# Kernel optimization log

Hardware: AMD Instinct MI355X
Metric: run time of the kernel (lower is better)

Reference implementation:

```python
import math
import jax, jax.numpy as jnp
import numpy as np

N_HEAD = 16

def setup_inputs() -> dict:
    key = jax.random.key(0)
    ks = jax.random.split(key, 3)
    B, T, C = 2, 2048, 1024
    x = jax.random.normal(ks[0], (B, T, C), dtype=jnp.float32)
    W_attn = jax.random.normal(ks[1], (3 * C, C), dtype=jnp.float32) * (1.0 / math.sqrt(C))
    b_attn = jnp.zeros((3 * C,), dtype=jnp.float32)
    W_proj = jax.random.normal(ks[2], (C, C), dtype=jnp.float32) * (1.0 / math.sqrt(C))
    b_proj = jnp.zeros((C,), dtype=jnp.float32)
    return {"x": x, "W_attn": W_attn, "b_attn": b_attn, "W_proj": W_proj, "b_proj": b_proj}

def reference(x, W_attn, b_attn, W_proj, b_proj):
    B, T, C = x.shape
    H = N_HEAD
    Dh = C // H
    qkv = x @ W_attn.T + b_attn                      # [B,T,3C]
    q, k, v = jnp.split(qkv, 3, axis=-1)
    q = q.reshape(B, T, H, Dh).transpose(0, 2, 1, 3)  # [B,H,T,Dh]
    k = k.reshape(B, T, H, Dh).transpose(0, 2, 1, 3)
    v = v.reshape(B, T, H, Dh).transpose(0, 2, 1, 3)
    att = jnp.einsum('bhqd,bhkd->bhqk', q, k) * (1.0 / math.sqrt(Dh))
    # ALiBi-style RPE: bias[h, r, c] = -(r - c) * 2^(-8/H * (h+1)) for c <= r, 0 above diag
    rows = jnp.arange(T)[:, None]
    cols = jnp.arange(T)[None, :]
    dist = jnp.minimum((cols - rows).astype(jnp.float32), 0.0)  # [T,T]
    slopes = 2.0 ** (-8.0 / H * (jnp.arange(H, dtype=jnp.float32) + 1.0))  # [H]
    att = att + slopes[None, :, None, None] * dist[None, None]
    causal = cols <= rows                              # [T,T]
    att = jnp.where(causal[None, None], att, -jnp.inf)
    att = jax.nn.softmax(att, axis=-1)                 # dropout p=0.0 -> identity
    y = jnp.einsum('bhqk,bhkd->bhqd', att, v)          # [B,H,T,Dh]
    y = y.transpose(0, 2, 1, 3).reshape(B, T, C)
    y = y @ W_proj.T + b_proj
    return y
```

## Files before the change

### kernel.cpp

```cpp
#include <hip/hip_runtime.h>

typedef __bf16 bf16x8 __attribute__((ext_vector_type(8)));
typedef __bf16 bf16x4 __attribute__((ext_vector_type(4)));
typedef float  f32x4  __attribute__((ext_vector_type(4)));
typedef float  f32x16 __attribute__((ext_vector_type(16)));

#define TSEQ 2048
#define CDIM 1024
#define NHEAD 16
#define DH 64
#define SCALE2 0.1803368801111137f

__device__ __forceinline__ void gl_lds16(const void* g, void* l) {
  __builtin_amdgcn_global_load_lds(
      (const __attribute__((address_space(1))) unsigned int*)g,
      (__attribute__((address_space(3))) unsigned int*)l, 16, 0, 0);
}

__device__ __forceinline__ float fexp2(float x) { return __builtin_amdgcn_exp2f(x); }

__device__ __forceinline__ unsigned cvtpk(float a, float b) {
  unsigned r;
  asm("v_cvt_pk_bf16_f32 %0, %1, %2" : "=v"(r) : "v"(a), "v"(b));
  return r;
}
__device__ __forceinline__ void permswap(unsigned& x, unsigned& y) {
  asm("v_permlane32_swap_b32 %0, %1" : "+v"(x), "+v"(y));
}

__device__ __forceinline__ float tsum16(const f32x16& s) {
  float a0 = s[0] + s[1], a1 = s[2] + s[3], a2 = s[4] + s[5], a3 = s[6] + s[7];
  float a4 = s[8] + s[9], a5 = s[10] + s[11], a6 = s[12] + s[13], a7 = s[14] + s[15];
  float b0 = a0 + a1, b1 = a2 + a3, b2 = a4 + a5, b3 = a6 + a7;
  return (b0 + b1) + (b2 + b3);
}

__global__ __launch_bounds__(256) void cvt_bf16_all(
    const float* __restrict__ x, const float* __restrict__ wa,
    const float* __restrict__ wp, __bf16* __restrict__ xb,
    __bf16* __restrict__ wab, __bf16* __restrict__ wpb) {
  int i = blockIdx.x * 256 + threadIdx.x;
  const float* in;
  __bf16* out;
  int off;
  if (i < 524288)      { in = x;  out = xb;  off = i; }
  else if (i < 917504) { in = wa; out = wab; off = i - 524288; }
  else                 { in = wp; out = wpb; off = i - 917504; }
  const float4* p = (const float4*)(in + (size_t)off * 8);
  float4 a = p[0], b = p[1];
  bf16x8 r;
  r[0] = (__bf16)a.x; r[1] = (__bf16)a.y; r[2] = (__bf16)a.z; r[3] = (__bf16)a.w;
  r[4] = (__bf16)b.x; r[5] = (__bf16)b.y; r[6] = (__bf16)b.z; r[7] = (__bf16)b.w;
  *(bf16x8*)(out + (size_t)off * 8) = r;
}

__global__ __launch_bounds__(256) void gemm_qkv(
    const __bf16* __restrict__ A, const __bf16* __restrict__ Bw,
    const float* __restrict__ bias,
    __bf16* __restrict__ q_buf, __bf16* __restrict__ k_buf,
    __bf16* __restrict__ vT_buf, int K) {
  __shared__ alignas(16) __bf16 lda[128 * 64];
  __shared__ alignas(16) __bf16 ldb[128 * 64];
  const int tid = threadIdx.x;
  const int lane = tid & 63, wid = tid >> 6;
  const int wm = wid >> 1, wn = wid & 1;
  const int row0 = blockIdx.y * 128, col0 = blockIdx.x * 128;
  f32x4 acc[4][4] = {};

  const int srow = lane >> 3;
  const int scb = ((lane & 7) ^ (lane >> 3)) * 16;

  for (int k0 = 0; k0 < K; k0 += 64) {
#pragma unroll
    for (int j = 0; j < 4; ++j) {
      int blk = j * 4 + wid;
      int r = blk * 8 + srow;
      char* la = (char*)lda + blk * 1024;
      char* lb = (char*)ldb + blk * 1024;
      gl_lds16((const char*)(A + (size_t)(row0 + r) * K + k0) + scb, la);
      gl_lds16((const char*)(Bw + (size_t)(col0 + r) * K + k0) + scb, lb);
    }
    __syncthreads();
#pragma unroll
    for (int kk = 0; kk < 2; ++kk) {
      const int sl = (((kk << 2) | (lane >> 4)) ^ (lane & 7)) * 16;
      bf16x8 af[4], bfr[4];
#pragma unroll
      for (int m = 0; m < 4; ++m)
        af[m] = *(const bf16x8*)((const char*)lda +
                                 (wm * 64 + m * 16 + (lane & 15)) * 128 + sl);
#pragma unroll
      for (int n = 0; n < 4; ++n)
        bfr[n] = *(const bf16x8*)((const char*)ldb +
                                  (wn * 64 + n * 16 + (lane & 15)) * 128 + sl);
#pragma unroll
      for (int m = 0; m < 4; ++m)
#pragma unroll
        for (int n = 0; n < 4; ++n)
          acc[m][n] = __builtin_amdgcn_mfma_f32_16x16x32_bf16(af[m], bfr[n], acc[m][n], 0, 0, 0);
    }
    __syncthreads();
  }
#pragma unroll
  for (int m = 0; m < 4; ++m) {
#pragma unroll
    for (int n = 0; n < 4; ++n) {
#pragma unroll
      for (int i = 0; i < 4; ++i) {
        int r = row0 + wm * 64 + m * 16 + (lane >> 4) * 4 + i;
        int c = col0 + wn * 64 + n * 16 + (lane & 15);
        float v = acc[m][n][i] + bias[c];
        int bb = r >> 11, t = r & 2047;
        int sec = c >> 10, cc = c & 1023;
        int hh = cc >> 6, d = cc & 63;
        size_t bh = (size_t)bb * NHEAD + hh;
        if (sec == 0)      q_buf[(bh * TSEQ + (size_t)t) * DH + d] = (__bf16)(v * SCALE2);
        else if (sec == 1) k_buf[(bh * TSEQ + (size_t)t) * DH + d] = (__bf16)v;
        else               vT_buf[(bh * DH + (size_t)d) * TSEQ + t] = (__bf16)v;
      }
    }
  }
}

__global__ __launch_bounds__(256) void gemm_proj(
    const __bf16* __restrict__ A, const __bf16* __restrict__ Bw,
    const float* __restrict__ bias, float* __restrict__ outf) {
  const int K = CDIM, N = CDIM;
  __shared__ alignas(16) __bf16 lda[64 * 64];
  __shared__ alignas(16) __bf16 ldb[128 * 64];
  const int tid = threadIdx.x;
  const int lane = tid & 63, wid = tid >> 6;
  const int row0 = blockIdx.y * 64, col0 = blockIdx.x * 128;
  f32x4 acc[4][2] = {};

  const int srow = lane >> 3;
  const int scb = ((lane & 7) ^ (lane >> 3)) * 16;

  for (int k0 = 0; k0 < K; k0 += 64) {
#pragma unroll
    for (int j = 0; j < 2; ++j) {
      int blk = j * 4 + wid;
      gl_lds16((const char*)(A + (size_t)(row0 + blk * 8 + srow) * K + k0) + scb,
               (char*)lda + blk * 1024);
    }
#pragma unroll
    for (int j = 0; j < 4; ++j) {
      int blk = j * 4 + wid;
      gl_lds16((const char*)(Bw + (size_t)(col0 + blk * 8 + srow) * K + k0) + scb,
               (char*)ldb + blk * 1024);
    }
    __syncthreads();
#pragma unroll
    for (int kk = 0; kk < 2; ++kk) {
      const int sl = (((kk << 2) | (lane >> 4)) ^ (lane & 7)) * 16;
      bf16x8 af[4], bfr[2];
#pragma unroll
      for (int m = 0; m < 4; ++m)
        af[m] = *(const bf16x8*)((const char*)lda + (m * 16 + (lane & 15)) * 128 + sl);
#pragma unroll
      for (int n = 0; n < 2; ++n)
        bfr[n] = *(const bf16x8*)((const char*)ldb +
                                  (wid * 32 + n * 16 + (lane & 15)) * 128 + sl);
#pragma unroll
      for (int m = 0; m < 4; ++m)
#pragma unroll
        for (int n = 0; n < 2; ++n)
          acc[m][n] = __builtin_amdgcn_mfma_f32_16x16x32_bf16(af[m], bfr[n], acc[m][n], 0, 0, 0);
    }
    __syncthreads();
  }
#pragma unroll
  for (int m = 0; m < 4; ++m) {
#pragma unroll
    for (int n = 0; n < 2; ++n) {
#pragma unroll
      for (int i = 0; i < 4; ++i) {
        int r = row0 + m * 16 + (lane >> 4) * 4 + i;
        int c = col0 + wid * 32 + n * 16 + (lane & 15);
        outf[(size_t)r * N + c] = acc[m][n][i] + bias[c];
      }
    }
  }
}

__device__ __forceinline__ void softmax_pv(
    f32x16& s, bool domask, int lq, int hi,
    float& l_r, f32x16& o0, f32x16& o1,
    const bf16x8* va0, const bf16x8* va1) {
#pragma unroll
  for (int r = 0; r < 16; ++r) s[r] = fexp2(s[r]);
  if (domask) {
#pragma unroll
    for (int r = 0; r < 16; ++r) {
      int kof = (r & 3) + 8 * (r >> 2) + 4 * hi;
      if (kof > lq) s[r] = 0.f;
    }
  }
  l_r += tsum16(s);
  bf16x8 pb[2];
#pragma unroll
  for (int kh = 0; kh < 2; ++kh) {
    const int bq = kh * 8;
    unsigned w0 = cvtpk(s[bq + 0], s[bq + 1]);
    unsigned w1 = cvtpk(s[bq + 2], s[bq + 3]);
    unsigned w2 = cvtpk(s[bq + 4], s[bq + 5]);
    unsigned w3 = cvtpk(s[bq + 6], s[bq + 7]);
    permswap(w0, w2);
    permswap(w1, w3);
    union { unsigned u[4]; bf16x8 v; } pbu;
    pbu.u[0] = w0; pbu.u[1] = w1; pbu.u[2] = w2; pbu.u[3] = w3;
    pb[kh] = pbu.v;
  }
  o0 = __builtin_amdgcn_mfma_f32_32x32x16_bf16(va0[0], pb[0], o0, 0, 0, 0);
  o0 = __builtin_amdgcn_mfma_f32_32x32x16_bf16(va0[1], pb[1], o0, 0, 0, 0);
  o1 = __builtin_amdgcn_mfma_f32_32x32x16_bf16(va1[0], pb[0], o1, 0, 0, 0);
  o1 = __builtin_amdgcn_mfma_f32_32x32x16_bf16(va1[1], pb[1], o1, 0, 0, 0);
}

__global__ __launch_bounds__(64) void attn_fwd(
    const __bf16* __restrict__ q_buf, const __bf16* __restrict__ k_buf,
    const __bf16* __restrict__ vT_buf, __bf16* __restrict__ y_buf) {
  const int lane = threadIdx.x;
  const int lq = lane & 31;
  const int hi = lane >> 5;
  const int bh = blockIdx.x;
  const int wv = blockIdx.y;
  const int b = bh >> 4, h = bh & 15;
  const int cH = 63 - wv, cL = wv;
  const float slope2 = exp2f(-0.5f * (float)(h + 1)) * 1.44269504f;
  const __bf16* qp = q_buf + (size_t)bh * TSEQ * DH;
  const __bf16* kp = k_buf + (size_t)bh * TSEQ * DH;
  const __bf16* vp = vT_buf + (size_t)bh * DH * TSEQ;

  bf16x8 qfH[4], qfL[4];
#pragma unroll
  for (int m = 0; m < 4; ++m) {
    qfH[m] = *(const bf16x8*)&qp[(size_t)(cH * 32 + lq) * DH + m * 16 + hi * 8];
    qfL[m] = *(const bf16x8*)&qp[(size_t)(cL * 32 + lq) * DH + m * 16 + hi * 8];
  }
  float pk_[16];
#pragma unroll
  for (int r = 0; r < 16; ++r)
    pk_[r] = slope2 * (float)((r & 3) + 8 * (r >> 2) + 4 * hi);

  f32x16 oH0 = {}, oH1 = {}, oL0 = {}, oL1 = {};
  float lH = 0.f, lL = 0.f;

  bf16x8 kf[4];
#pragma unroll
  for (int m = 0; m < 4; ++m)
    kf[m] = *(const bf16x8*)&kp[(size_t)lq * DH + m * 16 + hi * 8];

  for (int j = 0; j <= cH; ++j) {
    const int kt = j * 32;
    bf16x8 va0[2], va1[2];
#pragma unroll
    for (int kh = 0; kh < 2; ++kh) {
      va0[kh] = *(const bf16x8*)&vp[(size_t)lq * TSEQ + kt + kh * 16 + hi * 8];
      va1[kh] = *(const bf16x8*)&vp[(size_t)(32 + lq) * TSEQ + kt + kh * 16 + hi * 8];
    }
    bf16x8 kn[4];
    const bool pre = (j < cH);
    if (pre) {
#pragma unroll
      for (int m = 0; m < 4; ++m)
        kn[m] = *(const bf16x8*)&kp[(size_t)(kt + 32 + lq) * DH + m * 16 + hi * 8];
    }
    const float bH = slope2 * (float)(kt - cH * 32);
    f32x16 sH;
#pragma unroll
    for (int r = 0; r < 16; ++r) sH[r] = pk_[r] + bH;
#pragma unroll
    for (int m = 0; m < 4; ++m)
      sH = __builtin_amdgcn_mfma_f32_32x32x16_bf16(kf[m], qfH[m], sH, 0, 0, 0);
    const bool lact = (j <= cL);
    f32x16 sL;
    if (lact) {
      const float bL = slope2 * (float)(kt - cL * 32);
#pragma unroll
      for (int r = 0; r < 16; ++r) sL[r] = pk_[r] + bL;
#pragma unroll
      for (int m = 0; m < 4; ++m)
        sL = __builtin_amdgcn_mfma_f32_32x32x16_bf16(kf[m], qfL[m], sL, 0, 0, 0);
    }
    softmax_pv(sH, j == cH, lq, hi, lH, oH0, oH1, va0, va1);
    if (lact)
      softmax_pv(sL, j == cL, lq, hi, lL, oL0, oL1, va0, va1);
    if (pre) {
#pragma unroll
      for (int m = 0; m < 4; ++m) kf[m] = kn[m];
    }
  }
  lH += __shfl_xor(lH, 32, 64);
  lL += __shfl_xor(lL, 32, 64);

#pragma unroll
  for (int g2 = 0; g2 < 2; ++g2) {
    const int c = g2 ? cL : cH;
    const f32x16& a0 = g2 ? oL0 : oH0;
    const f32x16& a1 = g2 ? oL1 : oH1;
    const float inv = 1.0f / (g2 ? lL : lH);
    __bf16* yb = y_buf + ((size_t)b * TSEQ + c * 32 + lq) * CDIM + h * DH;
#pragma unroll
    for (int g = 0; g < 4; ++g) {
      bf16x4 v0, v1;
#pragma unroll
      for (int e = 0; e < 4; ++e) {
        v0[e] = (__bf16)(a0[4 * g + e] * inv);
        v1[e] = (__bf16)(a1[4 * g + e] * inv);
      }
      *(bf16x4*)&yb[8 * g + 4 * hi] = v0;
      *(bf16x4*)&yb[32 + 8 * g + 4 * hi] = v1;
    }
  }
}

extern "C" void kernel_launch(void* const* d_in, const int* in_sizes, int n_in,
                              void* d_out, int out_size, void* d_ws, size_t ws_size,
                              hipStream_t stream) {
  const float* x      = (const float*)d_in[0];
  const float* W_attn = (const float*)d_in[1];
  const float* b_attn = (const float*)d_in[2];
  const float* W_proj = (const float*)d_in[3];
  const float* b_proj = (const float*)d_in[4];
  float* out = (float*)d_out;
  char* ws = (char*)d_ws;
  const size_t MB = (size_t)1 << 20;
  __bf16* xb  = (__bf16*)(ws + 0 * MB);
  __bf16* wab = (__bf16*)(ws + 8 * MB);
  __bf16* wpb = (__bf16*)(ws + 14 * MB);
  __bf16* qbf = (__bf16*)(ws + 16 * MB);
  __bf16* kbf = (__bf16*)(ws + 24 * MB);
  __bf16* vtb = (__bf16*)(ws + 32 * MB);
  __bf16* yb  = (__bf16*)(ws + 40 * MB);

  cvt_bf16_all<<<4096, 256, 0, stream>>>(x, W_attn, W_proj, xb, wab, wpb);

  gemm_qkv<<<dim3(24, 32), 256, 0, stream>>>(xb, wab, b_attn, qbf, kbf, vtb, 1024);
  attn_fwd<<<dim3(32, 32), 64, 0, stream>>>(qbf, kbf, vtb, yb);
  gemm_proj<<<dim3(8, 64), 256, 0, stream>>>(yb, wpb, b_proj, out);
}
```

Baseline: 123.8 us.

## Split attention KV loop across two workgroups and add a combine kernel

Each attention workgroup now handles only even or odd key tiles, which doubles the grid to raise occupancy and parallelism. Unnormalized partial outputs and row sums are written to scratch space (d_out and the xb workspace region), and a new combine kernel adds the two halves and normalizes into y. The approach appears to skip a running max and relies on the fixed ALiBi/causal bias, so summing raw exp partials is valid. The cost is an extra kernel launch, a second round-trip of the partials through memory, and bf16 rounding of the partials before they are summed.

```diff
diff --git a/kernel.cpp b/kernel.cpp
--- a/kernel.cpp
+++ b/kernel.cpp
@@ -219,13 +219,15 @@
 
 __global__ __launch_bounds__(64) void attn_fwd(
     const __bf16* __restrict__ q_buf, const __bf16* __restrict__ k_buf,
-    const __bf16* __restrict__ vT_buf, __bf16* __restrict__ y_buf) {
+    const __bf16* __restrict__ vT_buf, __bf16* __restrict__ o_part,
+    float* __restrict__ l_part) {
   const int lane = threadIdx.x;
   const int lq = lane & 31;
   const int hi = lane >> 5;
   const int bh = blockIdx.x;
-  const int wv = blockIdx.y;
-  const int b = bh >> 4, h = bh & 15;
+  const int wv = blockIdx.y >> 1;
+  const int hf = blockIdx.y & 1;
+  const int h = bh & 15;
   const int cH = 63 - wv, cL = wv;
   const float slope2 = exp2f(-0.5f * (float)(h + 1)) * 1.44269504f;
   const __bf16* qp = q_buf + (size_t)bh * TSEQ * DH;
@@ -249,22 +251,15 @@
   bf16x8 kf[4];
 #pragma unroll
   for (int m = 0; m < 4; ++m)
-    kf[m] = *(const bf16x8*)&kp[(size_t)lq * DH + m * 16 + hi * 8];
-
-  for (int j = 0; j <= cH; ++j) {
+    kf[m] = *(const bf16x8*)&kp[(size_t)(hf * 32 + lq) * DH + m * 16 + hi * 8];
+
+  for (int j = hf; j <= cH; j += 2) {
     const int kt = j * 32;
     bf16x8 va0[2], va1[2];
 #pragma unroll
     for (int kh = 0; kh < 2; ++kh) {
       va0[kh] = *(const bf16x8*)&vp[(size_t)lq * TSEQ + kt + kh * 16 + hi * 8];
       va1[kh] = *(const bf16x8*)&vp[(size_t)(32 + lq) * TSEQ + kt + kh * 16 + hi * 8];
-    }
-    bf16x8 kn[4];
-    const bool pre = (j < cH);
-    if (pre) {
-#pragma unroll
-      for (int m = 0; m < 4; ++m)
-        kn[m] = *(const bf16x8*)&kp[(size_t)(kt + 32 + lq) * DH + m * 16 + hi * 8];
     }
     const float bH = slope2 * (float)(kt - cH * 32);
     f32x16 sH;
@@ -283,13 +278,14 @@
       for (int m = 0; m < 4; ++m)
         sL = __builtin_amdgcn_mfma_f32_32x32x16_bf16(kf[m], qfL[m], sL, 0, 0, 0);
     }
+    if (j + 2 <= cH) {
+#pragma unroll
+      for (int m = 0; m < 4; ++m)
+        kf[m] = *(const bf16x8*)&kp[(size_t)(kt + 64 + lq) * DH + m * 16 + hi * 8];
+    }
     softmax_pv(sH, j == cH, lq, hi, lH, oH0, oH1, va0, va1);
     if (lact)
       softmax_pv(sL, j == cL, lq, hi, lL, oL0, oL1, va0, va1);
-    if (pre) {
-#pragma unroll
-      for (int m = 0; m < 4; ++m) kf[m] = kn[m];
-    }
   }
   lH += __shfl_xor(lH, 32, 64);
   lL += __shfl_xor(lL, 32, 64);
@@ -299,20 +295,44 @@
     const int c = g2 ? cL : cH;
     const f32x16& a0 = g2 ? oL0 : oH0;
     const f32x16& a1 = g2 ? oL1 : oH1;
-    const float inv = 1.0f / (g2 ? lL : lH);
-    __bf16* yb = y_buf + ((size_t)b * TSEQ + c * 32 + lq) * CDIM + h * DH;
+    const float lv = g2 ? lL : lH;
+    const size_t slot = (size_t)hf * 2048 + (size_t)bh * 64 + c;
+    __bf16* op = o_part + slot * 2048 + (size_t)lq * 64;
 #pragma unroll
     for (int g = 0; g < 4; ++g) {
       bf16x4 v0, v1;
 #pragma unroll
       for (int e = 0; e < 4; ++e) {
-        v0[e] = (__bf16)(a0[4 * g + e] * inv);
-        v1[e] = (__bf16)(a1[4 * g + e] * inv);
+        v0[e] = (__bf16)a0[4 * g + e];
+        v1[e] = (__bf16)a1[4 * g + e];
       }
-      *(bf16x4*)&yb[8 * g + 4 * hi] = v0;
-      *(bf16x4*)&yb[32 + 8 * g + 4 * hi] = v1;
-    }
-  }
+      *(bf16x4*)&op[8 * g + 4 * hi] = v0;
+      *(bf16x4*)&op[32 + 8 * g + 4 * hi] = v1;
+    }
+    if (hi == 0) l_part[slot * 32 + lq] = lv;
+  }
+}
+
+__global__ __launch_bounds__(256) void attn_combine(
+    const __bf16* __restrict__ o_part, const float* __restrict__ lp,
+    __bf16* __restrict__ y_buf) {
+  const int tid = threadIdx.x;
+  const int t8 = tid & 7, rloc = tid >> 3;
+  const int row = blockIdx.x * 32 + rloc;
+  const int slot = row >> 5, lq = row & 31;
+  const int bh = slot >> 6, cc = slot & 63;
+  const int b = bh >> 4, h = bh & 15;
+  float l0 = lp[(size_t)slot * 32 + lq];
+  float l1 = lp[(size_t)(2048 + slot) * 32 + lq];
+  float inv = 1.0f / (l0 + l1);
+  bf16x8 a = *(const bf16x8*)(o_part + (size_t)slot * 2048 + (size_t)lq * 64 + t8 * 8);
+  bf16x8 c2 = *(const bf16x8*)(o_part + (size_t)(2048 + slot) * 2048 + (size_t)lq * 64 + t8 * 8);
+  bf16x8 r;
+#pragma unroll
+  for (int e = 0; e < 8; ++e)
+    r[e] = (__bf16)(((float)a[e] + (float)c2[e]) * inv);
+  const int t = cc * 32 + lq;
+  *(bf16x8*)&y_buf[((size_t)b * TSEQ + t) * CDIM + h * DH + t8 * 8] = r;
 }
 
 extern "C" void kernel_launch(void* const* d_in, const int* in_sizes, int n_in,
@@ -333,10 +353,13 @@
   __bf16* kbf = (__bf16*)(ws + 24 * MB);
   __bf16* vtb = (__bf16*)(ws + 32 * MB);
   __bf16* yb  = (__bf16*)(ws + 40 * MB);
+  float*  lpt = (float*)(ws + 0 * MB);
+  __bf16* opart = (__bf16*)d_out;
 
   cvt_bf16_all<<<4096, 256, 0, stream>>>(x, W_attn, W_proj, xb, wab, wpb);
 
   gemm_qkv<<<dim3(24, 32), 256, 0, stream>>>(xb, wab, b_attn, qbf, kbf, vtb, 1024);
-  attn_fwd<<<dim3(32, 32), 64, 0, stream>>>(qbf, kbf, vtb, yb);
+  attn_fwd<<<dim3(32, 64), 64, 0, stream>>>(qbf, kbf, vtb, opart, lpt);
+  attn_combine<<<2048, 256, 0, stream>>>(opart, lpt, yb);
   gemm_proj<<<dim3(8, 64), 256, 0, stream>>>(yb, wpb, b_proj, out);
 }
```

After: 128.3 us. +3.6%, slower.

## Pack Q/K/V in MFMA fragment order so attention loads are contiguous per wave

Applied to the files above, without the earlier changes.

The QKV GEMM epilogue now writes Q, K and V into a packed layout where each 32-row by 16-column MFMA operand fragment occupies a contiguous 1 KB block, indexed by lane*8. The attention kernel then loads each fragment as one fully coalesced 16-byte-per-lane read instead of strided row reads, which matters most for the previously transposed V reads spanning 2048-element rows. The cost is more scattered 2-byte stores in the GEMM epilogue.

```diff
diff --git a/kernel.cpp b/kernel.cpp
--- a/kernel.cpp
+++ b/kernel.cpp
@@ -57,8 +57,8 @@
 __global__ __launch_bounds__(256) void gemm_qkv(
     const __bf16* __restrict__ A, const __bf16* __restrict__ Bw,
     const float* __restrict__ bias,
-    __bf16* __restrict__ q_buf, __bf16* __restrict__ k_buf,
-    __bf16* __restrict__ vT_buf, int K) {
+    __bf16* __restrict__ q_pack, __bf16* __restrict__ k_pack,
+    __bf16* __restrict__ v_pack, int K) {
   __shared__ alignas(16) __bf16 lda[128 * 64];
   __shared__ alignas(16) __bf16 ldb[128 * 64];
   const int tid = threadIdx.x;
@@ -114,9 +114,17 @@
         int sec = c >> 10, cc = c & 1023;
         int hh = cc >> 6, d = cc & 63;
         size_t bh = (size_t)bb * NHEAD + hh;
-        if (sec == 0)      q_buf[(bh * TSEQ + (size_t)t) * DH + d] = (__bf16)(v * SCALE2);
-        else if (sec == 1) k_buf[(bh * TSEQ + (size_t)t) * DH + d] = (__bf16)v;
-        else               vT_buf[(bh * DH + (size_t)d) * TSEQ + t] = (__bf16)v;
+        if (sec == 2) {
+          int j = t >> 5, kh = (t >> 4) & 1, half = d >> 5;
+          int l2 = (d & 31) + ((t >> 3) & 1) * 32, e = t & 7;
+          v_pack[(bh * 256 + (size_t)(j * 4 + kh * 2 + half)) * 512 + l2 * 8 + e] = (__bf16)v;
+        } else {
+          int ch = t >> 5, mm = d >> 4;
+          int l2 = (t & 31) + ((d >> 3) & 1) * 32, e = d & 7;
+          size_t idx = ((bh * 64 + ch) * 4 + (size_t)mm) * 512 + l2 * 8 + e;
+          if (sec == 0) q_pack[idx] = (__bf16)(v * SCALE2);
+          else          k_pack[idx] = (__bf16)v;
+        }
       }
     }
   }
@@ -218,8 +226,8 @@
 }
 
 __global__ __launch_bounds__(64) void attn_fwd(
-    const __bf16* __restrict__ q_buf, const __bf16* __restrict__ k_buf,
-    const __bf16* __restrict__ vT_buf, __bf16* __restrict__ y_buf) {
+    const __bf16* __restrict__ q_pack, const __bf16* __restrict__ k_pack,
+    const __bf16* __restrict__ v_pack, __bf16* __restrict__ y_buf) {
   const int lane = threadIdx.x;
   const int lq = lane & 31;
   const int hi = lane >> 5;
@@ -228,15 +236,16 @@
   const int b = bh >> 4, h = bh & 15;
   const int cH = 63 - wv, cL = wv;
   const float slope2 = exp2f(-0.5f * (float)(h + 1)) * 1.44269504f;
-  const __bf16* qp = q_buf + (size_t)bh * TSEQ * DH;
-  const __bf16* kp = k_buf + (size_t)bh * TSEQ * DH;
-  const __bf16* vp = vT_buf + (size_t)bh * DH * TSEQ;
+  const __bf16* qpk = q_pack + (size_t)bh * 64 * 2048;
+  const __bf16* kpk = k_pack + (size_t)bh * 64 * 2048;
+  const __bf16* vpk = v_pack + (size_t)bh * 64 * 2048;
+  const int lo = lane * 8;
 
   bf16x8 qfH[4], qfL[4];
 #pragma unroll
   for (int m = 0; m < 4; ++m) {
-    qfH[m] = *(const bf16x8*)&qp[(size_t)(cH * 32 + lq) * DH + m * 16 + hi * 8];
-    qfL[m] = *(const bf16x8*)&qp[(size_t)(cL * 32 + lq) * DH + m * 16 + hi * 8];
+    qfH[m] = *(const bf16x8*)&qpk[(size_t)(cH * 4 + m) * 512 + lo];
+    qfL[m] = *(const bf16x8*)&qpk[(size_t)(cL * 4 + m) * 512 + lo];
   }
   float pk_[16];
 #pragma unroll
@@ -249,22 +258,22 @@
   bf16x8 kf[4];
 #pragma unroll
   for (int m = 0; m < 4; ++m)
-    kf[m] = *(const bf16x8*)&kp[(size_t)lq * DH + m * 16 + hi * 8];
+    kf[m] = *(const bf16x8*)&kpk[(size_t)m * 512 + lo];
 
   for (int j = 0; j <= cH; ++j) {
     const int kt = j * 32;
     bf16x8 va0[2], va1[2];
 #pragma unroll
     for (int kh = 0; kh < 2; ++kh) {
-      va0[kh] = *(const bf16x8*)&vp[(size_t)lq * TSEQ + kt + kh * 16 + hi * 8];
-      va1[kh] = *(const bf16x8*)&vp[(size_t)(32 + lq) * TSEQ + kt + kh * 16 + hi * 8];
+      va0[kh] = *(const bf16x8*)&vpk[(size_t)(j * 4 + kh * 2 + 0) * 512 + lo];
+      va1[kh] = *(const bf16x8*)&vpk[(size_t)(j * 4 + kh * 2 + 1) * 512 + lo];
     }
     bf16x8 kn[4];
     const bool pre = (j < cH);
     if (pre) {
 #pragma unroll
       for (int m = 0; m < 4; ++m)
-        kn[m] = *(const bf16x8*)&kp[(size_t)(kt + 32 + lq) * DH + m * 16 + hi * 8];
+        kn[m] = *(const bf16x8*)&kpk[(size_t)((j + 1) * 4 + m) * 512 + lo];
     }
     const float bH = slope2 * (float)(kt - cH * 32);
     f32x16 sH;
@@ -329,14 +338,14 @@
   __bf16* xb  = (__bf16*)(ws + 0 * MB);
   __bf16* wab = (__bf16*)(ws + 8 * MB);
   __bf16* wpb = (__bf16*)(ws + 14 * MB);
-  __bf16* qbf = (__bf16*)(ws + 16 * MB);
-  __bf16* kbf = (__bf16*)(ws + 24 * MB);
-  __bf16* vtb = (__bf16*)(ws + 32 * MB);
+  __bf16* qpk = (__bf16*)(ws + 16 * MB);
+  __bf16* kpk = (__bf16*)(ws + 24 * MB);
+  __bf16* vpk = (__bf16*)(ws + 32 * MB);
   __bf16* yb  = (__bf16*)(ws + 40 * MB);
 
   cvt_bf16_all<<<4096, 256, 0, stream>>>(x, W_attn, W_proj, xb, wab, wpb);
 
-  gemm_qkv<<<dim3(24, 32), 256, 0, stream>>>(xb, wab, b_attn, qbf, kbf, vtb, 1024);
-  attn_fwd<<<dim3(32, 32), 64, 0, stream>>>(qbf, kbf, vtb, yb);
+  gemm_qkv<<<dim3(24, 32), 256, 0, stream>>>(xb, wab, b_attn, qpk, kpk, vpk, 1024);
+  attn_fwd<<<dim3(32, 32), 64, 0, stream>>>(qpk, kpk, vpk, yb);
   gemm_proj<<<dim3(8, 64), 256, 0, stream>>>(yb, wpb, b_proj, out);
 }
```

After: 114.5 us. -7.6%, faster.
